# Kernel tuning notes

Measured on AMD Instinct MI355X. Metric: run time of the kernel, lower is better.

The kernel has to match this reference:

```python
import jax, jax.numpy as jnp
import numpy as np

N_HEADS = 16
NEG_INF = float('-inf')


def setup_inputs() -> dict:
    key = jax.random.key(0)
    ks = jax.random.split(key, 8)
    B, S, D = 8, 1024, 1024
    inp = {
        'q': jax.random.normal(ks[0], (B, S, D), jnp.float32),
        'k': jax.random.normal(ks[1], (B, S, D), jnp.float32),
        'v': jax.random.normal(ks[2], (B, S, D), jnp.float32),
        'key_padding_mask': jnp.zeros((B, S), bool),
        'Wq': jax.random.normal(ks[3], (D, D), jnp.float32) / np.sqrt(D),
        'bq': jnp.zeros((D,), jnp.float32),
        'Wk': jax.random.normal(ks[4], (D, D), jnp.float32) / np.sqrt(D),
        'bk': jnp.zeros((D,), jnp.float32),
        'Wv': jax.random.normal(ks[5], (D, D), jnp.float32) / np.sqrt(D),
        'bv': jnp.zeros((D,), jnp.float32),
        'Wo': jax.random.normal(ks[6], (D, D), jnp.float32) / np.sqrt(D),
        'bo': jnp.zeros((D,), jnp.float32),
    }
    return inp


def reference(q, k, v, key_padding_mask, Wq, bq, Wk, bk, Wv, bv, Wo, bo):
    B, T, D = q.shape
    S = k.shape[1]
    H = N_HEADS
    dh = D // H
    causal = True

    # projections (torch Linear: x @ W.T + b)
    qh = (q @ Wq.T + bq).reshape(B, T, H, dh).transpose(0, 2, 1, 3)  # b h t d
    kh = (k @ Wk.T + bk).reshape(B, S, H, dh).transpose(0, 2, 1, 3)  # b h s d
    vh = (v @ Wv.T + bv).reshape(B, S, H, dh).transpose(0, 2, 1, 3)  # b h s d

    s = jnp.einsum('bhtd,bhsd->bhts', qh, kh) / jnp.sqrt(jnp.asarray(dh, s_dtype(qh)))
    s = jnp.where(key_padding_mask[:, None, None, :], NEG_INF, s)
    if causal:
        cmask = jnp.triu(jnp.full((T, S), NEG_INF, s.dtype), 1)
        s = s + cmask[None, None]
    a = jax.nn.softmax(s.astype(jnp.float32), axis=-1).astype(s.dtype)
    o = jnp.einsum('bhts,bhsd->bhtd', a, vh)
    o = o.transpose(0, 2, 1, 3).reshape(B, T, D)
    return o @ Wo.T + bo


def s_dtype(x):
    return x.dtype
```

## Files before the change

kernel.cpp:

```cpp
#include <hip/hip_runtime.h>
#include <hip/hip_bf16.h>

typedef unsigned short u16;
typedef unsigned int u32;
typedef __attribute__((ext_vector_type(8))) short bf16x8;
typedef __attribute__((ext_vector_type(4))) float f32x4;

#define LOG2E 1.44269504088896340736f
#define QSCALE (0.125f * LOG2E)


__device__ inline u16 f2bf(float f) {
  union { float f; u32 u; } v; v.f = f;
  u32 r = v.u + 0x7fffu + ((v.u >> 16) & 1u);
  return (u16)(r >> 16);
}

__device__ inline void gload_lds16(const void* g, void* l) {
  __builtin_amdgcn_global_load_lds(
      (const __attribute__((address_space(1))) u32*)g,
      (__attribute__((address_space(3))) u32*)l, 16, 0, 0);
}

template<int CTRL>
__device__ inline float dppmov(float x) {
  int i = __builtin_bit_cast(int, x);
  int r = __builtin_amdgcn_update_dpp(i, i, CTRL, 0xf, 0xf, false);
  return __builtin_bit_cast(float, r);
}
__device__ inline float rowmax16(float v) {
  v = fmaxf(v, dppmov<0x128>(v));
  v = fmaxf(v, dppmov<0x124>(v));
  v = fmaxf(v, dppmov<0x122>(v));
  v = fmaxf(v, dppmov<0x121>(v));
  return v;
}
__device__ inline float rowsum16(float v) {
  v += dppmov<0x128>(v);
  v += dppmov<0x124>(v);
  v += dppmov<0x122>(v);
  v += dppmov<0x121>(v);
  return v;
}


__global__ void cvt_multi(const float4* __restrict__ s0, const float4* __restrict__ s1,
                          const float4* __restrict__ s2, const float4* __restrict__ s3,
                          ushort4* __restrict__ d0, ushort4* __restrict__ d1,
                          ushort4* __restrict__ d2, ushort4* __restrict__ d3, int n4) {
  const float4* s; ushort4* d;
  switch (blockIdx.y) {
    case 0: s = s0; d = d0; break;
    case 1: s = s1; d = d1; break;
    case 2: s = s2; d = d2; break;
    default: s = s3; d = d3; break;
  }
  int stride = gridDim.x * blockDim.x;
  for (int i = blockIdx.x * blockDim.x + threadIdx.x; i < n4; i += stride) {
    float4 v = s[i];
    ushort4 o;
    o.x = f2bf(v.x); o.y = f2bf(v.y); o.z = f2bf(v.z); o.w = f2bf(v.w);
    d[i] = o;
  }
}


__global__ void mask_flags(const unsigned char* __restrict__ mask,
                           unsigned char* __restrict__ flags) {
  int t = threadIdx.x;
  if (t >= 128) return;
  const uint4* p = (const uint4*)(mask + (size_t)t * 64);
  uint4 a = p[0], b = p[1], c = p[2], d = p[3];
  u32 v = a.x | a.y | a.z | a.w | b.x | b.y | b.z | b.w |
          c.x | c.y | c.z | c.w | d.x | d.y | d.z | d.w;
  flags[t] = v ? 1 : 0;
}


__global__ __launch_bounds__(512) void gemm_qkv(
    const u16* __restrict__ Aq, const u16* __restrict__ Ak, const u16* __restrict__ Av,
    const u16* __restrict__ Wqb, const u16* __restrict__ Wkb, const u16* __restrict__ Wvb,
    const float* __restrict__ bqp, const float* __restrict__ bkp, const float* __restrict__ bvp,
    u16* __restrict__ Qh, u16* __restrict__ Kh, u16* __restrict__ Vt,
    int M, int N, int K) {
  constexpr int BK = 32;
  __shared__ u16 sA[2][256 * BK];
  __shared__ u16 sB[2][128 * BK];

  const int nxy = gridDim.x * gridDim.y;
  const int nwg = nxy * gridDim.z;
  const int hw = blockIdx.z * nxy + blockIdx.y * gridDim.x + blockIdx.x;
  const int per = nwg >> 3;
  const int lg = (hw & 7) * per + (hw >> 3);
  const int z = lg >> 8;
  const int rem = lg & 255;
  const int m0 = (rem >> 3) * 256;
  const int n0 = (rem & 7) * 128;

  const u16* A  = (z == 0) ? Aq : (z == 1) ? Ak : Av;
  const u16* Bt = (z == 0) ? Wqb : (z == 1) ? Wkb : Wvb;
  const float* bias = (z == 0) ? bqp : (z == 1) ? bkp : bvp;

  const int tid = threadIdx.x;
  const int lane = tid & 63;
  const int wave = tid >> 6;
  const int g = lane >> 4;
  const int r = lane & 15;
  const int wr = wave >> 1;
  const int wc = wave & 1;

  f32x4 acc[4][4] = {};

  auto stage = [&](int buf, int kt) {
    const int k0 = kt * BK;
#pragma unroll
    for (int i = 0; i < 2; ++i) {
      int c = tid + i * 512;
      int row = c >> 2, cc = c & 3;
      gload_lds16(A + (size_t)(m0 + row) * K + k0 + cc * 8, &sA[buf][0] + c * 8);
    }
    {
      int c = tid;
      int row = c >> 2, cc = c & 3;
      gload_lds16(Bt + (size_t)(n0 + row) * K + k0 + cc * 8, &sB[buf][0] + c * 8);
    }
  };

  auto compute = [&](int buf) {
    const u16* aB = &sA[buf][0];
    const u16* bB = &sB[buf][0];
    bf16x8 avf[4], bvf[4];
#pragma unroll
    for (int i = 0; i < 4; ++i) {
      avf[i] = *(const bf16x8*)(aB + (wr * 64 + i * 16 + r) * BK + g * 8);
      bvf[i] = *(const bf16x8*)(bB + (wc * 64 + i * 16 + r) * BK + g * 8);
    }
#pragma unroll
    for (int i = 0; i < 4; ++i)
#pragma unroll
      for (int j = 0; j < 4; ++j)
        acc[i][j] = __builtin_amdgcn_mfma_f32_16x16x32_bf16(avf[i], bvf[j], acc[i][j], 0, 0, 0);
  };

  stage(0, 0);
  const int NT = K / BK;
  for (int kt = 0; kt < NT; ++kt) {
    __syncthreads();
    if (kt + 1 < NT) stage((kt + 1) & 1, kt + 1);
    compute(kt & 1);
  }

#pragma unroll
  for (int i = 0; i < 4; ++i) {
    int rowb = m0 + wr * 64 + i * 16 + g * 4;
#pragma unroll
    for (int j = 0; j < 4; ++j) {
      int col = n0 + wc * 64 + j * 16 + r;
      float bv = bias[col];
#pragma unroll
      for (int q = 0; q < 4; ++q) {
        int row = rowb + q;
        float v = acc[i][j][q] + bv;
        int b = row >> 10, t = row & 1023, h = col >> 6, d = col & 63;
        if (z == 0) {
          Qh[((((size_t)b * 16 + h) << 10) + t) * 64 + d] = f2bf(v * QSCALE);
        } else if (z == 1) {
          Kh[((((size_t)b * 16 + h) << 10) + t) * 64 + d] = f2bf(v);
        } else {
          Vt[(((size_t)b * 16 + h) * 64 + d) * 1024 + t] = f2bf(v);
        }
      }
    }
  }
}


__global__ __launch_bounds__(512) void gemm_o(
    const u16* __restrict__ A, const u16* __restrict__ Bt,
    const float* __restrict__ bias, float* __restrict__ Cout,
    int M, int N, int K) {
  constexpr int BK = 32;
  __shared__ u16 sA[2][256 * BK];
  __shared__ u16 sB[2][128 * BK];

  const int nwg = gridDim.x * gridDim.y;
  const int hw = blockIdx.y * gridDim.x + blockIdx.x;
  const int per = nwg >> 3;
  const int lg = (hw & 7) * per + (hw >> 3);
  const int m0 = (lg >> 3) * 256;
  const int n0 = (lg & 7) * 128;

  const int tid = threadIdx.x;
  const int lane = tid & 63;
  const int wave = tid >> 6;
  const int g = lane >> 4;
  const int r = lane & 15;
  const int wr = wave >> 1, wc = wave & 1;

  f32x4 acc[4][4] = {};

  auto stage = [&](int buf, int kt) {
    const int k0 = kt * BK;
#pragma unroll
    for (int i = 0; i < 2; ++i) {
      int c = tid + i * 512;
      int row = c >> 2, cc = c & 3;
      gload_lds16(A + (size_t)(m0 + row) * K + k0 + cc * 8, &sA[buf][0] + c * 8);
    }
    {
      int c = tid;
      int row = c >> 2, cc = c & 3;
      gload_lds16(Bt + (size_t)(n0 + row) * K + k0 + cc * 8, &sB[buf][0] + c * 8);
    }
  };

  auto compute = [&](int buf) {
    const u16* aB = &sA[buf][0];
    const u16* bB = &sB[buf][0];
    bf16x8 avf[4], bvf[4];
#pragma unroll
    for (int i = 0; i < 4; ++i) {
      avf[i] = *(const bf16x8*)(aB + (wr * 64 + i * 16 + r) * BK + g * 8);
      bvf[i] = *(const bf16x8*)(bB + (wc * 64 + i * 16 + r) * BK + g * 8);
    }
#pragma unroll
    for (int i = 0; i < 4; ++i)
#pragma unroll
      for (int j = 0; j < 4; ++j)
        acc[i][j] = __builtin_amdgcn_mfma_f32_16x16x32_bf16(avf[i], bvf[j], acc[i][j], 0, 0, 0);
  };

  stage(0, 0);
  const int NT = K / BK;
  for (int kt = 0; kt < NT; ++kt) {
    __syncthreads();
    if (kt + 1 < NT) stage((kt + 1) & 1, kt + 1);
    compute(kt & 1);
  }

#pragma unroll
  for (int i = 0; i < 4; ++i) {
    int rowb = m0 + wr * 64 + i * 16 + g * 4;
#pragma unroll
    for (int j = 0; j < 4; ++j) {
      int col = n0 + wc * 64 + j * 16 + r;
      float bv = bias[col];
#pragma unroll
      for (int q = 0; q < 4; ++q) {
        int row = rowb + q;
        Cout[(size_t)row * N + col] = acc[i][j][q] + bv;
      }
    }
  }
}


__global__ __launch_bounds__(256) void attn_fwd(
    const u16* __restrict__ Qh, const u16* __restrict__ Kh,
    const u16* __restrict__ Vt, const unsigned char* __restrict__ mask,
    const unsigned char* __restrict__ padflags,
    u16* __restrict__ O) {
  constexpr int S = 1024, DH = 64;
  __shared__ u16 sK[2][64 * 64];
  __shared__ u16 sV[2][64 * 64];
  __shared__ u16 sP[4][16 * 64];

  const int tid = threadIdx.x, lane = tid & 63, wave = tid >> 6;
  const int g = lane >> 4, r = lane & 15;
  const int bh = blockIdx.x;
  const int qt = (int)gridDim.y - 1 - (int)blockIdx.y;
  const int b = bh >> 4, h = bh & 15;
  const int qw = qt * 128 + wave * 32;

  bf16x8 qf[2][2];
#pragma unroll
  for (int u = 0; u < 2; ++u) {
    const u16* Qb = Qh + ((size_t)bh * S + qw + u * 16 + r) * DH;
    qf[u][0] = *(const bf16x8*)(Qb + g * 8);
    qf[u][1] = *(const bf16x8*)(Qb + 32 + g * 8);
  }

  f32x4 acc[2][4] = {};
  float mrun[2][4], lrun[2][4];
#pragma unroll
  for (int u = 0; u < 2; ++u)
#pragma unroll
    for (int i = 0; i < 4; ++i) { mrun[u][i] = -INFINITY; lrun[u][i] = 0.f; }

  auto stage = [&](int buf, int kvt) {
    const int s0k = kvt * 64;
#pragma unroll
    for (int i = 0; i < 2; ++i) {
      int c = tid + i * 256;
      int row = c >> 3;
      int cc = (c & 7) ^ (row & 7);
      gload_lds16(Kh + ((size_t)bh * S + s0k + row) * DH + cc * 8, &sK[buf][0] + c * 8);
      gload_lds16(Vt + ((size_t)bh * DH + row) * S + s0k + cc * 8, &sV[buf][0] + c * 8);
    }
  };

  const int NT = 2 * (qt + 1);
  stage(0, 0);
  for (int kvt = 0; kvt < NT; ++kvt) {
    __syncthreads();
    if (kvt + 1 < NT) stage((kvt + 1) & 1, kvt + 1);
    const int cur = kvt & 1;
    const int s0 = kvt * 64;
    const bool pad = padflags[b * 16 + (s0 >> 6)] != 0;
    const u16* Kb = &sK[cur][0];
    const u16* Vb = &sV[cur][0];
    u16* Pw = &sP[wave][0];

#pragma unroll
    for (int u = 0; u < 2; ++u) {
      const int qg = qw + u * 16;
      if (s0 > qg + 15) continue;
      const bool diag = (s0 + 63 > qg);

      f32x4 sc[4] = {};
#pragma unroll
      for (int ss = 0; ss < 4; ++ss) {
#pragma unroll
        for (int kc = 0; kc < 2; ++kc) {
          int krow = ss * 16 + r;
          int byteoff = krow * 128 + kc * 64 + g * 16;
          bf16x8 kf = *(const bf16x8*)((const char*)Kb + (byteoff ^ ((krow & 7) << 4)));
          sc[ss] = __builtin_amdgcn_mfma_f32_16x16x32_bf16(qf[u][kc], kf, sc[ss], 0, 0, 0);
        }
      }

      float sv[4][4];
      float pmax[4] = {-INFINITY, -INFINITY, -INFINITY, -INFINITY};
#pragma unroll
      for (int ss = 0; ss < 4; ++ss) {
        float padd = 0.f;
        if (pad) {
          int s_g = s0 + ss * 16 + r;
          if (mask[(size_t)b * S + s_g]) padd = -INFINITY;
        }
#pragma unroll
        for (int reg = 0; reg < 4; ++reg) {
          float v = sc[ss][reg] + padd;
          if (diag) {
            int s_g = s0 + ss * 16 + r;
            int q_g = qg + g * 4 + reg;
            if (s_g > q_g) v = -INFINITY;
          }
          sv[ss][reg] = v;
          pmax[reg] = fmaxf(pmax[reg], v);
        }
      }
#pragma unroll
      for (int reg = 0; reg < 4; ++reg) {
        float m = rowmax16(pmax[reg]);
        float newm = fmaxf(mrun[u][reg], m);
        float alpha = (newm == -INFINITY) ? 1.f : exp2f(mrun[u][reg] - newm);
        mrun[u][reg] = newm;
        float rs = 0.f;
#pragma unroll
        for (int ss = 0; ss < 4; ++ss) {
          float p = (newm == -INFINITY) ? 0.f : exp2f(sv[ss][reg] - newm);
          sv[ss][reg] = p;
          rs += p;
        }
        rs = rowsum16(rs);
        lrun[u][reg] = lrun[u][reg] * alpha + rs;
#pragma unroll
        for (int df = 0; df < 4; ++df) acc[u][df][reg] *= alpha;
      }

#pragma unroll
      for (int ss = 0; ss < 4; ++ss) {
#pragma unroll
        for (int reg = 0; reg < 4; ++reg) {
          int qrow = g * 4 + reg;
          int byteoff = qrow * 128 + (ss * 16 + r) * 2;
          u32 bits = __builtin_bit_cast(u32, sv[ss][reg]);
          *(u16*)((char*)Pw + (byteoff ^ ((qrow & 7) << 4))) = (u16)(bits >> 16);
        }
      }

#pragma unroll
      for (int sc2 = 0; sc2 < 2; ++sc2) {
        int pbyte = r * 128 + sc2 * 64 + g * 16;
        bf16x8 pf = *(const bf16x8*)((const char*)Pw + (pbyte ^ ((r & 7) << 4)));
#pragma unroll
        for (int df = 0; df < 4; ++df) {
          int vrow = df * 16 + r;
          int vbyte = vrow * 128 + sc2 * 64 + g * 16;
          bf16x8 vf = *(const bf16x8*)((const char*)Vb + (vbyte ^ ((vrow & 7) << 4)));
          acc[u][df] = __builtin_amdgcn_mfma_f32_16x16x32_bf16(pf, vf, acc[u][df], 0, 0, 0);
        }
      }
    }
  }

#pragma unroll
  for (int u = 0; u < 2; ++u) {
#pragma unroll
    for (int reg = 0; reg < 4; ++reg) {
      float l = lrun[u][reg];
      float inv = (l > 0.f) ? 1.f / l : 0.f;
      int t = qw + u * 16 + g * 4 + reg;
#pragma unroll
      for (int df = 0; df < 4; ++df) {
        float vo = acc[u][df][reg] * inv;
        O[((size_t)b * 1024 + t) * 1024 + h * 64 + df * 16 + r] = f2bf(vo);
      }
    }
  }
}


extern "C" void kernel_launch(void* const* d_in, const int* in_sizes, int n_in,
                              void* d_out, int out_size, void* d_ws, size_t ws_size,
                              hipStream_t stream) {
  const float* q  = (const float*)d_in[0];
  const float* k  = (const float*)d_in[1];
  const float* v  = (const float*)d_in[2];
  const unsigned char* mask = (const unsigned char*)d_in[3];
  const float* Wq = (const float*)d_in[4];
  const float* bq = (const float*)d_in[5];
  const float* Wk = (const float*)d_in[6];
  const float* bk = (const float*)d_in[7];
  const float* Wv = (const float*)d_in[8];
  const float* bv = (const float*)d_in[9];
  const float* Wo = (const float*)d_in[10];
  const float* bo = (const float*)d_in[11];

  const int M = 8192, N = 1024, K = 1024;
  const size_t MB = 1u << 20;
  char* ws = (char*)d_ws;

  u16* Aq   = (u16*)(ws);
  u16* Ak   = (u16*)(ws + 16 * MB);
  u16* Av   = (u16*)(ws + 32 * MB);
  u16* Qh   = (u16*)(ws + 48 * MB);
  u16* Kh   = (u16*)(ws + 64 * MB);
  u16* Vt   = (u16*)(ws + 80 * MB);
  u16* Wqb  = (u16*)(ws + 96 * MB);
  u16* Wkb  = Wqb + (1u << 20);
  u16* Wvb  = Wkb + (1u << 20);
  u16* Wob  = Wvb + (1u << 20);
  unsigned char* flags = (unsigned char*)(ws + 104 * MB);
  u16* AttO = Aq;

  cvt_multi<<<dim3(1024, 3), 256, 0, stream>>>(
      (const float4*)q, (const float4*)k, (const float4*)v, (const float4*)q,
      (ushort4*)Aq, (ushort4*)Ak, (ushort4*)Av, (ushort4*)Aq, (M * K) / 4);
  cvt_multi<<<dim3(256, 4), 256, 0, stream>>>(
      (const float4*)Wq, (const float4*)Wk, (const float4*)Wv, (const float4*)Wo,
      (ushort4*)Wqb, (ushort4*)Wkb, (ushort4*)Wvb, (ushort4*)Wob, (N * K) / 4);
  mask_flags<<<1, 128, 0, stream>>>(mask, flags);

  gemm_qkv<<<dim3(8, 32, 3), 512, 0, stream>>>(
      Aq, Ak, Av, Wqb, Wkb, Wvb, bq, bk, bv, Qh, Kh, Vt, M, N, K);

  attn_fwd<<<dim3(128, 8), 256, 0, stream>>>(Qh, Kh, Vt, mask, flags, AttO);

  gemm_o<<<dim3(8, 32), 512, 0, stream>>>(
      AttO, Wob, bo, (float*)d_out, M, N, K);
}
```

Baseline: 239.0 us.

## Shrink GEMM tiles to 128x128, add lazy softmax rescale and MFMA priority

```diff
diff --git a/kernel.cpp b/kernel.cpp
--- a/kernel.cpp
+++ b/kernel.cpp
@@ -8,6 +8,7 @@
 
 #define LOG2E 1.44269504088896340736f
 #define QSCALE (0.125f * LOG2E)
+#define DEFER_THR 8.0f
 
 
 __device__ inline u16 f2bf(float f) {
@@ -77,24 +78,21 @@
 }
 
 
-__global__ __launch_bounds__(512) void gemm_qkv(
+__global__ __launch_bounds__(256) void gemm_qkv(
     const u16* __restrict__ Aq, const u16* __restrict__ Ak, const u16* __restrict__ Av,
     const u16* __restrict__ Wqb, const u16* __restrict__ Wkb, const u16* __restrict__ Wvb,
     const float* __restrict__ bqp, const float* __restrict__ bkp, const float* __restrict__ bvp,
     u16* __restrict__ Qh, u16* __restrict__ Kh, u16* __restrict__ Vt,
     int M, int N, int K) {
   constexpr int BK = 32;
-  __shared__ u16 sA[2][256 * BK];
+  __shared__ u16 sA[2][128 * BK];
   __shared__ u16 sB[2][128 * BK];
 
-  const int nxy = gridDim.x * gridDim.y;
-  const int nwg = nxy * gridDim.z;
-  const int hw = blockIdx.z * nxy + blockIdx.y * gridDim.x + blockIdx.x;
-  const int per = nwg >> 3;
-  const int lg = (hw & 7) * per + (hw >> 3);
-  const int z = lg >> 8;
-  const int rem = lg & 255;
-  const int m0 = (rem >> 3) * 256;
+  const int hw = blockIdx.z * 512 + blockIdx.y * 8 + blockIdx.x;
+  const int lg = (hw & 7) * 192 + (hw >> 3);
+  const int z = lg / 512;
+  const int rem = lg - z * 512;
+  const int m0 = (rem >> 3) * 128;
   const int n0 = (rem & 7) * 128;
 
   const u16* A  = (z == 0) ? Aq : (z == 1) ? Ak : Av;
@@ -106,8 +104,7 @@
   const int wave = tid >> 6;
   const int g = lane >> 4;
   const int r = lane & 15;
-  const int wr = wave >> 1;
-  const int wc = wave & 1;
+  const int wr = wave >> 1, wc = wave & 1;
 
   f32x4 acc[4][4] = {};
 
@@ -115,31 +112,16 @@
     const int k0 = kt * BK;
 #pragma unroll
     for (int i = 0; i < 2; ++i) {
-      int c = tid + i * 512;
+      int c = tid + i * 256;
       int row = c >> 2, cc = c & 3;
       gload_lds16(A + (size_t)(m0 + row) * K + k0 + cc * 8, &sA[buf][0] + c * 8);
     }
-    {
-      int c = tid;
+#pragma unroll
+    for (int i = 0; i < 2; ++i) {
+      int c = tid + i * 256;
       int row = c >> 2, cc = c & 3;
       gload_lds16(Bt + (size_t)(n0 + row) * K + k0 + cc * 8, &sB[buf][0] + c * 8);
     }
-  };
-
-  auto compute = [&](int buf) {
-    const u16* aB = &sA[buf][0];
-    const u16* bB = &sB[buf][0];
-    bf16x8 avf[4], bvf[4];
-#pragma unroll
-    for (int i = 0; i < 4; ++i) {
-      avf[i] = *(const bf16x8*)(aB + (wr * 64 + i * 16 + r) * BK + g * 8);
-      bvf[i] = *(const bf16x8*)(bB + (wc * 64 + i * 16 + r) * BK + g * 8);
-    }
-#pragma unroll
-    for (int i = 0; i < 4; ++i)
-#pragma unroll
-      for (int j = 0; j < 4; ++j)
-        acc[i][j] = __builtin_amdgcn_mfma_f32_16x16x32_bf16(avf[i], bvf[j], acc[i][j], 0, 0, 0);
   };
 
   stage(0, 0);
@@ -147,7 +129,19 @@
   for (int kt = 0; kt < NT; ++kt) {
     __syncthreads();
     if (kt + 1 < NT) stage((kt + 1) & 1, kt + 1);
-    compute(kt & 1);
+    const u16* a_base = &sA[kt & 1][0];
+    const u16* b_base = &sB[kt & 1][0];
+    bf16x8 avf[4], bvf[4];
+#pragma unroll
+    for (int i = 0; i < 4; ++i) {
+      avf[i] = *(const bf16x8*)(a_base + (wr * 64 + i * 16 + r) * BK + g * 8);
+      bvf[i] = *(const bf16x8*)(b_base + (wc * 64 + i * 16 + r) * BK + g * 8);
+    }
+#pragma unroll
+    for (int i = 0; i < 4; ++i)
+#pragma unroll
+      for (int j = 0; j < 4; ++j)
+        acc[i][j] = __builtin_amdgcn_mfma_f32_16x16x32_bf16(avf[i], bvf[j], acc[i][j], 0, 0, 0);
   }
 
 #pragma unroll
@@ -175,19 +169,17 @@
 }
 
 
-__global__ __launch_bounds__(512) void gemm_o(
+__global__ __launch_bounds__(256) void gemm_o(
     const u16* __restrict__ A, const u16* __restrict__ Bt,
     const float* __restrict__ bias, float* __restrict__ Cout,
     int M, int N, int K) {
   constexpr int BK = 32;
-  __shared__ u16 sA[2][256 * BK];
+  __shared__ u16 sA[2][128 * BK];
   __shared__ u16 sB[2][128 * BK];
 
-  const int nwg = gridDim.x * gridDim.y;
-  const int hw = blockIdx.y * gridDim.x + blockIdx.x;
-  const int per = nwg >> 3;
-  const int lg = (hw & 7) * per + (hw >> 3);
-  const int m0 = (lg >> 3) * 256;
+  const int hw = blockIdx.y * 8 + blockIdx.x;
+  const int lg = (hw & 7) * 64 + (hw >> 3);
+  const int m0 = (lg >> 3) * 128;
   const int n0 = (lg & 7) * 128;
 
   const int tid = threadIdx.x;
@@ -203,31 +195,16 @@
     const int k0 = kt * BK;
 #pragma unroll
     for (int i = 0; i < 2; ++i) {
-      int c = tid + i * 512;
+      int c = tid + i * 256;
       int row = c >> 2, cc = c & 3;
       gload_lds16(A + (size_t)(m0 + row) * K + k0 + cc * 8, &sA[buf][0] + c * 8);
     }
-    {
-      int c = tid;
+#pragma unroll
+    for (int i = 0; i < 2; ++i) {
+      int c = tid + i * 256;
       int row = c >> 2, cc = c & 3;
       gload_lds16(Bt + (size_t)(n0 + row) * K + k0 + cc * 8, &sB[buf][0] + c * 8);
     }
-  };
-
-  auto compute = [&](int buf) {
-    const u16* aB = &sA[buf][0];
-    const u16* bB = &sB[buf][0];
-    bf16x8 avf[4], bvf[4];
-#pragma unroll
-    for (int i = 0; i < 4; ++i) {
-      avf[i] = *(const bf16x8*)(aB + (wr * 64 + i * 16 + r) * BK + g * 8);
-      bvf[i] = *(const bf16x8*)(bB + (wc * 64 + i * 16 + r) * BK + g * 8);
-    }
-#pragma unroll
-    for (int i = 0; i < 4; ++i)
-#pragma unroll
-      for (int j = 0; j < 4; ++j)
-        acc[i][j] = __builtin_amdgcn_mfma_f32_16x16x32_bf16(avf[i], bvf[j], acc[i][j], 0, 0, 0);
   };
 
   stage(0, 0);
@@ -235,7 +212,19 @@
   for (int kt = 0; kt < NT; ++kt) {
     __syncthreads();
     if (kt + 1 < NT) stage((kt + 1) & 1, kt + 1);
-    compute(kt & 1);
+    const u16* a_base = &sA[kt & 1][0];
+    const u16* b_base = &sB[kt & 1][0];
+    bf16x8 avf[4], bvf[4];
+#pragma unroll
+    for (int i = 0; i < 4; ++i) {
+      avf[i] = *(const bf16x8*)(a_base + (wr * 64 + i * 16 + r) * BK + g * 8);
+      bvf[i] = *(const bf16x8*)(b_base + (wc * 64 + i * 16 + r) * BK + g * 8);
+    }
+#pragma unroll
+    for (int i = 0; i < 4; ++i)
+#pragma unroll
+      for (int j = 0; j < 4; ++j)
+        acc[i][j] = __builtin_amdgcn_mfma_f32_16x16x32_bf16(avf[i], bvf[j], acc[i][j], 0, 0, 0);
   }
 
 #pragma unroll
@@ -318,6 +307,7 @@
       const bool diag = (s0 + 63 > qg);
 
       f32x4 sc[4] = {};
+      __builtin_amdgcn_s_setprio(1);
 #pragma unroll
       for (int ss = 0; ss < 4; ++ss) {
 #pragma unroll
@@ -328,6 +318,7 @@
           sc[ss] = __builtin_amdgcn_mfma_f32_16x16x32_bf16(qf[u][kc], kf, sc[ss], 0, 0, 0);
         }
       }
+      __builtin_amdgcn_s_setprio(0);
 
       float sv[4][4];
       float pmax[4] = {-INFINITY, -INFINITY, -INFINITY, -INFINITY};
@@ -350,23 +341,44 @@
           pmax[reg] = fmaxf(pmax[reg], v);
         }
       }
-#pragma unroll
-      for (int reg = 0; reg < 4; ++reg) {
-        float m = rowmax16(pmax[reg]);
-        float newm = fmaxf(mrun[u][reg], m);
-        float alpha = (newm == -INFINITY) ? 1.f : exp2f(mrun[u][reg] - newm);
-        mrun[u][reg] = newm;
-        float rs = 0.f;
-#pragma unroll
-        for (int ss = 0; ss < 4; ++ss) {
-          float p = (newm == -INFINITY) ? 0.f : exp2f(sv[ss][reg] - newm);
-          sv[ss][reg] = p;
-          rs += p;
-        }
-        rs = rowsum16(rs);
-        lrun[u][reg] = lrun[u][reg] * alpha + rs;
-#pragma unroll
-        for (int df = 0; df < 4; ++df) acc[u][df][reg] *= alpha;
+
+      float tm[4];
+#pragma unroll
+      for (int reg = 0; reg < 4; ++reg) tm[reg] = rowmax16(pmax[reg]);
+      float dmax = fmaxf(fmaxf(tm[0] - mrun[u][0], tm[1] - mrun[u][1]),
+                         fmaxf(tm[2] - mrun[u][2], tm[3] - mrun[u][3]));
+      if (__any(dmax > DEFER_THR)) {
+#pragma unroll
+        for (int reg = 0; reg < 4; ++reg) {
+          float newm = fmaxf(mrun[u][reg], tm[reg]);
+          float alpha = (newm == -INFINITY) ? 1.f : exp2f(mrun[u][reg] - newm);
+          mrun[u][reg] = newm;
+          float rs = 0.f;
+#pragma unroll
+          for (int ss = 0; ss < 4; ++ss) {
+            float p = (newm == -INFINITY) ? 0.f : exp2f(sv[ss][reg] - newm);
+            sv[ss][reg] = p;
+            rs += p;
+          }
+          rs = rowsum16(rs);
+          lrun[u][reg] = lrun[u][reg] * alpha + rs;
+#pragma unroll
+          for (int df = 0; df < 4; ++df) acc[u][df][reg] *= alpha;
+        }
+      } else {
+#pragma unroll
+        for (int reg = 0; reg < 4; ++reg) {
+          float m = mrun[u][reg];
+          float rs = 0.f;
+#pragma unroll
+          for (int ss = 0; ss < 4; ++ss) {
+            float p = (m == -INFINITY) ? 0.f : exp2f(sv[ss][reg] - m);
+            sv[ss][reg] = p;
+            rs += p;
+          }
+          rs = rowsum16(rs);
+          lrun[u][reg] += rs;
+        }
       }
 
 #pragma unroll
@@ -380,6 +392,7 @@
         }
       }
 
+      __builtin_amdgcn_s_setprio(1);
 #pragma unroll
       for (int sc2 = 0; sc2 < 2; ++sc2) {
         int pbyte = r * 128 + sc2 * 64 + g * 16;
@@ -392,6 +405,7 @@
           acc[u][df] = __builtin_amdgcn_mfma_f32_16x16x32_bf16(pf, vf, acc[u][df], 0, 0, 0);
         }
       }
+      __builtin_amdgcn_s_setprio(0);
     }
   }
 
@@ -453,11 +467,11 @@
       (ushort4*)Wqb, (ushort4*)Wkb, (ushort4*)Wvb, (ushort4*)Wob, (N * K) / 4);
   mask_flags<<<1, 128, 0, stream>>>(mask, flags);
 
-  gemm_qkv<<<dim3(8, 32, 3), 512, 0, stream>>>(
+  gemm_qkv<<<dim3(8, 64, 3), 256, 0, stream>>>(
       Aq, Ak, Av, Wqb, Wkb, Wvb, bq, bk, bv, Qh, Kh, Vt, M, N, K);
 
   attn_fwd<<<dim3(128, 8), 256, 0, stream>>>(Qh, Kh, Vt, mask, flags, AttO);
 
-  gemm_o<<<dim3(8, 32), 512, 0, stream>>>(
+  gemm_o<<<dim3(8, 64), 256, 0, stream>>>(
       AttO, Wob, bo, (float*)d_out, M, N, K);
 }
```

Result: faster. 229.9 us (-3.8%).
